# Kernel optimization log

Measured on AMD Instinct MI355X. Metric: run time of the kernel, lower is better.

The kernel has to match this reference:

```python
import jax, jax.numpy as jnp
import numpy as np

B, T, D, H, DK = 4, 1024, 512, 8, 64
L = 2 * T - 1  # relative position length
EPS = 1e-3     # keras LayerNormalization default epsilon


def rel_shift(x, klen):
    # x: [B, H, T, L] with L = 2T-1 -> [B, H, T, klen] (Transformer-XL shift)
    b, h, t, l = x.shape
    x = x.reshape(b, h, l, t)[:, :, 1:, :]
    x = x.reshape(b, h, t, l - 1)
    return x[:, :, :, :klen]


def setup_inputs() -> dict:
    key = jax.random.key(0)
    ks = jax.random.split(key, 16)
    s = 0.02
    return {
        "x": jax.random.normal(ks[0], (B, T, D), jnp.float32),
        "pos": jax.random.normal(ks[1], (B, L, D), jnp.float32),
        "content_bias": jax.random.normal(ks[2], (H, DK), jnp.float32) * s,
        "pos_bias": jax.random.normal(ks[3], (H, DK), jnp.float32) * s,
        "gamma": jnp.ones((D,), jnp.float32),
        "beta": jnp.zeros((D,), jnp.float32),
        "Wq": jax.random.normal(ks[4], (D, H, DK), jnp.float32) * s,
        "bq": jnp.zeros((H, DK), jnp.float32),
        "Wk": jax.random.normal(ks[5], (D, H, DK), jnp.float32) * s,
        "bk": jnp.zeros((H, DK), jnp.float32),
        "Wv": jax.random.normal(ks[6], (D, H, DK), jnp.float32) * s,
        "bv": jnp.zeros((H, DK), jnp.float32),
        "Wp": jax.random.normal(ks[7], (D, H, DK), jnp.float32) * s,
        "Wo": jax.random.normal(ks[8], (H, DK, D), jnp.float32) * s,
        "bo": jnp.zeros((D,), jnp.float32),
    }


def reference(x, pos, content_bias, pos_bias, gamma, beta,
              Wq, bq, Wk, bk, Wv, bv, Wp, Wo, bo):
    # pre-norm LayerNorm
    mean = jnp.mean(x, axis=-1, keepdims=True)
    var = jnp.var(x, axis=-1, keepdims=True)
    y = (x - mean) * jax.lax.rsqrt(var + EPS) * gamma + beta

    # per-head projections
    q = jnp.einsum("bid,dhk->bihk", y, Wq) + bq      # [B,T,H,DK]
    k = jnp.einsum("bjd,dhk->bjhk", y, Wk) + bk
    v = jnp.einsum("bjd,dhk->bjhk", y, Wv) + bv
    p = jnp.einsum("bld,dhk->blhk", pos, Wp)          # [B,L,H,DK], no bias

    # Transformer-XL content + positional scores
    content = jnp.einsum("bihk,bjhk->bhij", q + content_bias, k)   # [B,H,T,T]
    positional = jnp.einsum("bihk,blhk->bhil", q + pos_bias, p)    # [B,H,T,L]
    positional = rel_shift(positional, content.shape[-1])          # [B,H,T,T]

    scores = (content + positional) / np.sqrt(DK).astype(np.float32)
    attn = jax.nn.softmax(scores, axis=-1)

    o = jnp.einsum("bhij,bjhk->bihk", attn, v)       # [B,T,H,DK]
    out = jnp.einsum("bihk,hkd->bid", o, Wo) + bo    # [B,T,D]

    # dropout is identity at inference; residual with factor=1.0
    return x + out
```

## Files before the change

### kernel.cpp

```cpp
#include <hip/hip_runtime.h>
#include <hip/hip_bf16.h>

typedef __hip_bfloat16 bf16;
typedef __attribute__((ext_vector_type(8))) short short8;
typedef __attribute__((ext_vector_type(4))) float f32x4;

#define B_  4
#define T_  1024
#define D_  512
#define H_  8
#define DK_ 64
#define L_  2047

__device__ __forceinline__ float b2f(bf16 v) { return __bfloat162float(v); }
__device__ __forceinline__ bf16  f2b(float v) { return __float2bfloat16(v); }
__device__ __forceinline__ float bits2f(unsigned short u) {
    return __uint_as_float(((unsigned int)u) << 16);
}
__device__ __forceinline__ unsigned short fbits(float v) {
    bf16 h = f2b(v); return *(unsigned short*)&h;
}

#define MFMA16(a, b, c) __builtin_amdgcn_mfma_f32_16x16x32_bf16(a, b, c, 0, 0, 0)
#define GLD_LDS16(g, l) __builtin_amdgcn_global_load_lds( \
    (const __attribute__((address_space(1))) unsigned int*)(g), \
    (__attribute__((address_space(3))) unsigned int*)(l), 16, 0, 0)

__global__ __launch_bounds__(256) void prep_all(
        const float* __restrict__ Wq, const float* __restrict__ Wk,
        const float* __restrict__ Wv, const float* __restrict__ Wp,
        const float* __restrict__ Wo,
        const float* __restrict__ bq, const float* __restrict__ bk,
        const float* __restrict__ bv,
        const float* __restrict__ pos, const float* __restrict__ x,
        const float* __restrict__ gamma, const float* __restrict__ beta,
        bf16* __restrict__ Wqkv_t, bf16* __restrict__ Wp_t, bf16* __restrict__ Wo_t,
        float* __restrict__ biasq, bf16* __restrict__ pos_bf, bf16* __restrict__ y) {
    __shared__ float tl[32][33];
    __shared__ float ws1[4], ws2[4];
    const int blk = blockIdx.x;
    const int t = threadIdx.x;

    if (blk < 1280) {
        const int z = blk >> 8, rem = blk & 255;
        const float* W; bf16* Wt; int roff;
        switch (z) {
            case 0: W = Wq; Wt = Wqkv_t; roff = 0;    break;
            case 1: W = Wk; Wt = Wqkv_t; roff = 512;  break;
            case 2: W = Wv; Wt = Wqkv_t; roff = 1024; break;
            case 3: W = Wp; Wt = Wp_t;   roff = 0;    break;
            default: W = Wo; Wt = Wo_t;  roff = 0;    break;
        }
        const int n0 = (rem & 15) * 32, k0 = (rem >> 4) * 32;
        const int tx = t & 31, ty = t >> 5;
#pragma unroll
        for (int r = 0; r < 4; ++r)
            tl[ty + r * 8][tx] = W[(size_t)(k0 + ty + r * 8) * 512 + n0 + tx];
        __syncthreads();
#pragma unroll
        for (int r = 0; r < 4; ++r)
            Wt[(size_t)(roff + n0 + ty + r * 8) * 512 + k0 + tx] = f2b(tl[tx][ty + r * 8]);
    } else if (blk < 1286) {
        int i = (blk - 1280) * 256 + t;
        biasq[i] = (i < 512) ? bq[i] : (i < 1024) ? bk[i - 512] : bv[i - 1024];
    } else if (blk < 3333) {
        size_t i = ((size_t)(blk - 1286) * 256 + t) * 8;
        float4 a = *(const float4*)(pos + i);
        float4 c = *(const float4*)(pos + i + 4);
        uint4 wv;
        wv.x = ((unsigned)fbits(a.y) << 16) | fbits(a.x);
        wv.y = ((unsigned)fbits(a.w) << 16) | fbits(a.z);
        wv.z = ((unsigned)fbits(c.y) << 16) | fbits(c.x);
        wv.w = ((unsigned)fbits(c.w) << 16) | fbits(c.z);
        *(uint4*)((unsigned short*)pos_bf + i) = wv;
    } else {
        const int row = blk - 3333;
        const float* xr = x + (size_t)row * D_;
        float v0 = xr[t];
        float v1 = xr[t + 256];
        float s  = v0 + v1;
        float s2 = v0 * v0 + v1 * v1;
#pragma unroll
        for (int off = 32; off > 0; off >>= 1) {
            s  += __shfl_down(s,  off, 64);
            s2 += __shfl_down(s2, off, 64);
        }
        const int wid = t >> 6, lane = t & 63;
        if (!lane) { ws1[wid] = s; ws2[wid] = s2; }
        __syncthreads();
        float S  = ws1[0] + ws1[1] + ws1[2] + ws1[3];
        float S2 = ws2[0] + ws2[1] + ws2[2] + ws2[3];
        float mean = S * (1.f / D_);
        float var  = S2 * (1.f / D_) - mean * mean;
        float r = rsqrtf(var + 1e-3f);
        bf16* yr = y + (size_t)row * D_;
        yr[t]       = f2b((v0 - mean) * r * gamma[t]       + beta[t]);
        yr[t + 256] = f2b((v1 - mean) * r * gamma[t + 256] + beta[t + 256]);
    }
}

template <bool C_F32>
__device__ __forceinline__ void gemm_body(
        const bf16* __restrict__ A, const bf16* __restrict__ Wt,
        const float* __restrict__ bias, const float* __restrict__ resid,
        void* __restrict__ Cv, int M, size_t seg_elems, int m0, int n0,
        unsigned short (*A_s)[32], unsigned short (*B_s)[32]) {
    const int t = threadIdx.x;
    const int w = t >> 6, lane = t & 63;
    const int quad = lane >> 4, n16 = lane & 15;
    const int wm = (w >> 1) * 64, wn = (w & 1) * 64;

    f32x4 acc[4][4];
#pragma unroll
    for (int a = 0; a < 4; ++a)
#pragma unroll
        for (int b = 0; b < 4; ++b) acc[a][b] = (f32x4){0.f, 0.f, 0.f, 0.f};

    const int ar = lane >> 2, ac8 = (lane & 3) * 8;
    auto stage = [&](int k0, int buf) {
        const int bo = buf << 7;
#pragma unroll
        for (int ps = 0; ps < 2; ++ps) {
            int br = (ps * 4 + w) * 16;
            GLD_LDS16(A  + (size_t)(m0 + br + ar) * 512 + k0 + ac8, &A_s[bo + br][0]);
            GLD_LDS16(Wt + (size_t)(n0 + br + ar) * 512 + k0 + ac8, &B_s[bo + br][0]);
        }
    };
    stage(0, 0);
    int cur = 0;
    for (int k0 = 0; k0 < 512; k0 += 32) {
        __syncthreads();
        if (k0 + 32 < 512) stage(k0 + 32, cur ^ 1);
        const int bo = cur << 7;
        short8 af[4], bfr[4];
#pragma unroll
        for (int i = 0; i < 4; ++i) {
            af[i]  = *(const short8*)&A_s[bo + wm + i * 16 + n16][quad * 8];
            bfr[i] = *(const short8*)&B_s[bo + wn + i * 16 + n16][quad * 8];
        }
#pragma unroll
        for (int mi = 0; mi < 4; ++mi)
#pragma unroll
            for (int ni = 0; ni < 4; ++ni)
                acc[mi][ni] = MFMA16(af[mi], bfr[ni], acc[mi][ni]);
        cur ^= 1;
    }

    const int seg = n0 >> 9;
#pragma unroll
    for (int mi = 0; mi < 4; ++mi) {
#pragma unroll
        for (int r = 0; r < 4; ++r) {
            int row = m0 + wm + mi * 16 + quad * 4 + r;
            if (row >= M) continue;
#pragma unroll
            for (int ni = 0; ni < 4; ++ni) {
                int col  = n0 + wn + ni * 16 + n16;
                int coll = col & 511;
                float vv = acc[mi][ni][r];
                if (bias) vv += bias[col];
                if constexpr (C_F32) {
                    float* C = (float*)Cv + seg * seg_elems;
                    if (resid) vv += resid[(size_t)row * 512 + coll];
                    C[(size_t)row * 512 + coll] = vv;
                } else {
                    bf16* C = (bf16*)Cv + seg * seg_elems;
                    C[(size_t)row * 512 + coll] = f2b(vv);
                }
            }
        }
    }
}

__global__ __launch_bounds__(256) void gemm_qkvp(
        const bf16* __restrict__ y, const bf16* __restrict__ pos_bf,
        const bf16* __restrict__ Wqkv_t, const bf16* __restrict__ Wp_t,
        const float* __restrict__ biasq,
        bf16* __restrict__ q, bf16* __restrict__ p, size_t seg_elems) {
    __shared__ __align__(16) unsigned short A_s[256][32];
    __shared__ __align__(16) unsigned short B_s[256][32];
    const int gid = blockIdx.x;
    if (gid < 384) {
        const int xcd = gid & 7, s = gid >> 3;
        const int n = s % 12;
        const int m = xcd * 4 + s / 12;
        gemm_body<false>(y, Wqkv_t, biasq, nullptr, q, 4096, seg_elems,
                         m * 128, n * 128, A_s, B_s);
    } else {
        const int g2 = gid - 384;
        const int xcd = g2 & 7, s = g2 >> 3;
        const int n = s & 3;
        const int m = xcd * 8 + (s >> 2);
        gemm_body<false>(pos_bf, Wp_t, nullptr, nullptr, p, 8188, 0,
                         m * 128, n * 128, A_s, B_s);
    }
}

__global__ __launch_bounds__(256) void gemm_out(
        const bf16* __restrict__ o, const bf16* __restrict__ Wo_t,
        const float* __restrict__ bo, const float* __restrict__ x,
        float* __restrict__ out) {
    __shared__ __align__(16) unsigned short A_s[256][32];
    __shared__ __align__(16) unsigned short B_s[256][32];
    const int xcd = blockIdx.x & 7, s = blockIdx.x >> 3;
    const int n = s & 3;
    const int m = xcd * 4 + (s >> 2);
    gemm_body<true>(o, Wo_t, bo, x, out, 4096, 0, m * 128, n * 128, A_s, B_s);
}

__global__ __launch_bounds__(256, 2) void attn_mfma_kernel(
        const bf16* __restrict__ q, const bf16* __restrict__ k,
        const bf16* __restrict__ v, const bf16* __restrict__ p,
        const float* __restrict__ cbias, const float* __restrict__ pbias,
        bf16* __restrict__ o) {
    __shared__ __align__(16) unsigned short k_s[2][4096];
    __shared__ __align__(16) unsigned short pw_s[2][8192];
    __shared__ __align__(16) unsigned short vt_s[2][64][72];
    __shared__ __align__(16) unsigned short gbuf[4][16][72];
    __shared__ float cb_s[64], pb_s[64];
    __shared__ float wrap_s;

    const int i0 = blockIdx.x * 64;
    const int h  = blockIdx.y;
    const int b  = blockIdx.z;
    const int t  = threadIdx.x;
    const int w    = t >> 6;
    const int lane = t & 63;
    const int quad = lane >> 4;
    const int n16  = lane & 15;
    const int h64  = h * 64;
    const float sc_scale = 0.125f * 1.4426950408889634f;

    if (t < 64)       cb_s[t]      = cbias[h64 + t];
    else if (t < 128) pb_s[t - 64] = pbias[h64 + t - 64];

    const int l8 = lane >> 3, l7 = lane & 7;
    const int clog8 = (l7 ^ l8) * 8;
    const unsigned short* ksrc[2];
    const unsigned short* psrc[4];
#pragma unroll
    for (int ps = 0; ps < 2; ++ps) {
        int row = (w * 2 + ps) * 8 + l8;
        ksrc[ps] = (const unsigned short*)k + ((size_t)(b * T_ + row) * 512 + h64 + clog8);
    }
    const int slb = T_ - i0 - 63;
#pragma unroll
    for (int ps = 0; ps < 4; ++ps) {
        int row = (w * 4 + ps) * 8 + l8;
        psrc[ps] = (const unsigned short*)p + ((size_t)(b * L_ + slb + row) * 512 + h64 + clog8);
    }
    auto stage = [&](int j0n, int nxt) {
        size_t joff = (size_t)j0n * 512;
#pragma unroll
        for (int ps = 0; ps < 2; ++ps)
            GLD_LDS16(ksrc[ps] + joff, &k_s[nxt][(w * 2 + ps) * 512]);
#pragma unroll
        for (int ps = 0; ps < 4; ++ps)
            GLD_LDS16(psrc[ps] + joff, &pw_s[nxt][(w * 4 + ps) * 512]);
    };

    const int vd2 = (t & 31) * 2, vjg = t >> 5;
    const unsigned short* vsrc = (const unsigned short*)v +
        ((size_t)(b * T_ + vjg * 8) * 512 + h64 + vd2);
    unsigned int vReg[8];
    auto vload = [&](int j0n) {
        const unsigned short* vg = vsrc + (size_t)j0n * 512;
#pragma unroll
        for (int e = 0; e < 8; ++e) vReg[e] = *(const unsigned int*)(vg + (size_t)e * 512);
    };
    auto vwrite = [&](int nxt) {
        uint4 wlo, whi;
        wlo.x = (vReg[0] & 0xffffu) | (vReg[1] << 16);
        wlo.y = (vReg[2] & 0xffffu) | (vReg[3] << 16);
        wlo.z = (vReg[4] & 0xffffu) | (vReg[5] << 16);
        wlo.w = (vReg[6] & 0xffffu) | (vReg[7] << 16);
        whi.x = (vReg[0] >> 16) | (vReg[1] & 0xffff0000u);
        whi.y = (vReg[2] >> 16) | (vReg[3] & 0xffff0000u);
        whi.z = (vReg[4] >> 16) | (vReg[5] & 0xffff0000u);
        whi.w = (vReg[6] >> 16) | (vReg[7] & 0xffff0000u);
        *(uint4*)&vt_s[nxt][vd2][vjg * 8]     = wlo;
        *(uint4*)&vt_s[nxt][vd2 + 1][vjg * 8] = whi;
    };

    stage(0, 0);
    vload(0);
    __syncthreads();

    short8 ac[2], ap[2];
    {
        const unsigned short* qrow = (const unsigned short*)q +
            ((size_t)(b * T_ + i0 + 16 * w + n16) * 512 + h64);
#pragma unroll
        for (int kc = 0; kc < 2; ++kc) {
            uint4 u = *(const uint4*)(qrow + kc * 32 + quad * 8);
            const unsigned short* uv = (const unsigned short*)&u;
            unsigned short* acp = (unsigned short*)&ac[kc];
            unsigned short* app = (unsigned short*)&ap[kc];
#pragma unroll
            for (int e = 0; e < 8; ++e) {
                int d = kc * 32 + quad * 8 + e;
                float qv = bits2f(uv[e]);
                acp[e] = fbits((qv + cb_s[d]) * sc_scale);
                app[e] = fbits((qv + pb_s[d]) * sc_scale);
            }
        }
    }
    if (i0 == 0 && t < 64) {
        float part = (b2f(q[(size_t)(b * T_ + 1) * 512 + h64 + t]) + pb_s[t]) *
                     b2f(p[(size_t)(b * L_) * 512 + h64 + t]);
#pragma unroll
        for (int m = 1; m < 64; m <<= 1) part += __shfl_xor(part, m, 64);
        if (t == 0) wrap_s = part * sc_scale;
    }

    int srcl[4]; bool hi_[4];
#pragma unroll
    for (int r = 0; r < 4; ++r) {
        int ii = quad * 4 + r;
        srcl[r] = (lane & 48) | ((n16 - ii - 1) & 15);
        hi_[r]  = n16 > ii;
    }
    short8 onesb;
    {
        const short ov = (n16 == 0) ? (short)0x3F80 : (short)0;
#pragma unroll
        for (int e = 0; e < 8; ++e) onesb[e] = ov;
    }

    const int pwoff = 48 - 16 * w;
    const int swzA  = (quad ^ (n16 & 7)) * 16;
    const int swzB  = swzA ^ 64;

    f32x4 O[4], O4;
#pragma unroll
    for (int nt = 0; nt < 4; ++nt) O[nt] = (f32x4){0.f, 0.f, 0.f, 0.f};
    O4 = (f32x4){0.f, 0.f, 0.f, 0.f};

    auto qk = [&](f32x4 (&Sc)[4], f32x4 (&G)[5], int buf) {
        const char* krA  = (const char*)&k_s[buf][0]  + n16 * 128 + swzA;
        const char* krB  = (const char*)&k_s[buf][0]  + n16 * 128 + swzB;
        const char* pwrA = (const char*)&pw_s[buf][0] + (pwoff + n16) * 128 + swzA;
        const char* pwrB = (const char*)&pw_s[buf][0] + (pwoff + n16) * 128 + swzB;
#pragma unroll
        for (int nt = 0; nt < 4; ++nt) Sc[nt] = (f32x4){0.f, 0.f, 0.f, 0.f};
#pragma unroll
        for (int ct = 0; ct < 5; ++ct) G[ct] = (f32x4){0.f, 0.f, 0.f, 0.f};
#pragma unroll
        for (int kc = 0; kc < 2; ++kc) {
#pragma unroll
            for (int nt = 0; nt < 4; ++nt) {
                short8 bk = *(const short8*)((kc ? krB : krA) + nt * 2048);
                Sc[nt] = MFMA16(ac[kc], bk, Sc[nt]);
            }
#pragma unroll
            for (int ct = 0; ct < 5; ++ct) {
                short8 bp = *(const short8*)((kc ? pwrB : pwrA) + ct * 2048);
                G[ct] = MFMA16(ap[kc], bp, G[ct]);
            }
        }
    };

    auto sm_pv = [&](const f32x4 (&Sc)[4], const f32x4 (&G)[5], int vb, bool dowrap) {
        float pe[4][4];
#pragma unroll
        for (int r = 0; r < 4; ++r) {
            float s0 = __shfl(G[0][r], srcl[r], 64);
            float s1 = __shfl(G[1][r], srcl[r], 64);
            float s2 = __shfl(G[2][r], srcl[r], 64);
            float s3 = __shfl(G[3][r], srcl[r], 64);
            float s4 = __shfl(G[4][r], srcl[r], 64);
            pe[0][r] = Sc[0][r] + (hi_[r] ? s1 : s0);
            pe[1][r] = Sc[1][r] + (hi_[r] ? s2 : s1);
            pe[2][r] = Sc[2][r] + (hi_[r] ? s3 : s2);
            pe[3][r] = Sc[3][r] + (hi_[r] ? s4 : s3);
        }
        if (dowrap && i0 == 0 && w == 0 && lane == 15)
            pe[3][0] = Sc[3][0] + wrap_s;
#pragma unroll
        for (int ct = 0; ct < 4; ++ct)
#pragma unroll
            for (int r = 0; r < 4; ++r)
                *(bf16*)&gbuf[w][quad * 4 + r][ct * 16 + n16] = f2b(exp2f(pe[ct][r]));
#pragma unroll
        for (int kc = 0; kc < 2; ++kc) {
            short8 pa = *(const short8*)&gbuf[w][n16][kc * 32 + quad * 8];
#pragma unroll
            for (int nt = 0; nt < 4; ++nt) {
                short8 vb8 = *(const short8*)&vt_s[vb][nt * 16 + n16][kc * 32 + quad * 8];
                O[nt] = MFMA16(pa, vb8, O[nt]);
            }
            O4 = MFMA16(pa, onesb, O4);
        }
    };

    f32x4 ScA[4], GA[5], ScB[4], GB[5];

    vwrite(0);
    stage(64, 1);
    vload(64);
    qk(ScA, GA, 0);

    auto body = [&](int tt, f32x4 (&ScC)[4], f32x4 (&GC)[5],
                    const f32x4 (&ScP)[4], const f32x4 (&GP)[5], bool more) {
        __syncthreads();
        vwrite(tt & 1);
        if (more) { stage((tt + 1) * 64, (tt + 1) & 1); vload((tt + 1) * 64); }
        qk(ScC, GC, tt & 1);
        sm_pv(ScP, GP, (tt - 1) & 1, false);
    };

#pragma unroll
    for (int tp = 0; tp < 7; ++tp) {
        body(2 * tp + 1, ScB, GB, ScA, GA, true);
        body(2 * tp + 2, ScA, GA, ScB, GB, true);
    }
    body(15, ScB, GB, ScA, GA, false);

    __syncthreads();
    sm_pv(ScB, GB, 1, true);

#pragma unroll
    for (int r = 0; r < 4; ++r) {
        float l = __shfl(O4[r], lane & 48, 64);
        float inv = 1.f / l;
        int row = i0 + 16 * w + quad * 4 + r;
#pragma unroll
        for (int nt = 0; nt < 4; ++nt)
            o[(size_t)(b * T_ + row) * 512 + h64 + nt * 16 + n16] = f2b(O[nt][r] * inv);
    }
}

extern "C" void kernel_launch(void* const* d_in, const int* in_sizes, int n_in,
                              void* d_out, int out_size, void* d_ws, size_t ws_size,
                              hipStream_t stream) {
    (void)in_sizes; (void)n_in; (void)out_size;
    const float* x     = (const float*)d_in[0];
    const float* pos   = (const float*)d_in[1];
    const float* cb    = (const float*)d_in[2];
    const float* pb    = (const float*)d_in[3];
    const float* gamma = (const float*)d_in[4];
    const float* beta  = (const float*)d_in[5];
    const float* Wq    = (const float*)d_in[6];
    const float* bq    = (const float*)d_in[7];
    const float* Wk    = (const float*)d_in[8];
    const float* bk    = (const float*)d_in[9];
    const float* Wv    = (const float*)d_in[10];
    const float* bv    = (const float*)d_in[11];
    const float* Wp    = (const float*)d_in[12];
    const float* Wo    = (const float*)d_in[13];
    const float* bo    = (const float*)d_in[14];
    float* out = (float*)d_out;

    const int BT = B_ * T_;

    const size_t sz_bt = (size_t)BT * D_;
    const size_t sz_bl = (size_t)(B_ * L_) * D_;
    const size_t sz_w  = 512 * 512;
    const size_t need  = (5 * sz_bt + sz_bl + 5 * sz_w) * sizeof(bf16) + 1536 * sizeof(float);
    if (ws_size < need) return;

    bf16* y       = (bf16*)d_ws;
    bf16* o       = y + sz_bt;
    bf16* q       = y + 2 * sz_bt;
    bf16* k       = y + 3 * sz_bt;
    bf16* v       = y + 4 * sz_bt;
    bf16* p       = y + 5 * sz_bt;
    bf16* Wqkv_t  = p + sz_bl;
    bf16* Wp_t    = Wqkv_t + 3 * sz_w;
    bf16* Wo_t    = Wp_t + sz_w;
    float* biasq  = (float*)(Wo_t + sz_w);
    bf16* pos_bf  = (bf16*)d_out;

    prep_all<<<7429, 256, 0, stream>>>(Wq, Wk, Wv, Wp, Wo, bq, bk, bv, pos, x,
                                       gamma, beta, Wqkv_t, Wp_t, Wo_t, biasq, pos_bf, y);

    gemm_qkvp<<<640, 256, 0, stream>>>(y, pos_bf, Wqkv_t, Wp_t, biasq, q, p, sz_bt);

    attn_mfma_kernel<<<dim3(T_ / 64, H_, B_), 256, 0, stream>>>(q, k, v, p, cb, pb, o);

    gemm_out<<<128, 256, 0, stream>>>(o, Wo_t, bo, x, out);
}
```

Measured before the change: 208.4 us.

## Reuse overlapping positional tiles via ring buffer, retile output GEMM, add MFMA priority

Result: faster. 185.7 us (-10.9%).

```diff
diff --git a/kernel.cpp b/kernel.cpp
--- a/kernel.cpp
+++ b/kernel.cpp
@@ -99,11 +99,10 @@
     }
 }
 
-template <bool C_F32>
 __device__ __forceinline__ void gemm_body(
         const bf16* __restrict__ A, const bf16* __restrict__ Wt,
-        const float* __restrict__ bias, const float* __restrict__ resid,
-        void* __restrict__ Cv, int M, size_t seg_elems, int m0, int n0,
+        const float* __restrict__ bias,
+        bf16* __restrict__ C, int M, size_t seg_elems, int m0, int n0,
         unsigned short (*A_s)[32], unsigned short (*B_s)[32]) {
     const int t = threadIdx.x;
     const int w = t >> 6, lane = t & 63;
@@ -159,14 +158,8 @@
                 int coll = col & 511;
                 float vv = acc[mi][ni][r];
                 if (bias) vv += bias[col];
-                if constexpr (C_F32) {
-                    float* C = (float*)Cv + seg * seg_elems;
-                    if (resid) vv += resid[(size_t)row * 512 + coll];
-                    C[(size_t)row * 512 + coll] = vv;
-                } else {
-                    bf16* C = (bf16*)Cv + seg * seg_elems;
-                    C[(size_t)row * 512 + coll] = f2b(vv);
-                }
+                bf16* Cp = C + seg * seg_elems;
+                Cp[(size_t)row * 512 + coll] = f2b(vv);
             }
         }
     }
@@ -184,15 +177,13 @@
         const int xcd = gid & 7, s = gid >> 3;
         const int n = s % 12;
         const int m = xcd * 4 + s / 12;
-        gemm_body<false>(y, Wqkv_t, biasq, nullptr, q, 4096, seg_elems,
-                         m * 128, n * 128, A_s, B_s);
+        gemm_body(y, Wqkv_t, biasq, q, 4096, seg_elems, m * 128, n * 128, A_s, B_s);
     } else {
         const int g2 = gid - 384;
         const int xcd = g2 & 7, s = g2 >> 3;
         const int n = s & 3;
         const int m = xcd * 8 + (s >> 2);
-        gemm_body<false>(pos_bf, Wp_t, nullptr, nullptr, p, 8188, 0,
-                         m * 128, n * 128, A_s, B_s);
+        gemm_body(pos_bf, Wp_t, nullptr, p, 8188, 0, m * 128, n * 128, A_s, B_s);
     }
 }
 
@@ -200,12 +191,64 @@
         const bf16* __restrict__ o, const bf16* __restrict__ Wo_t,
         const float* __restrict__ bo, const float* __restrict__ x,
         float* __restrict__ out) {
-    __shared__ __align__(16) unsigned short A_s[256][32];
+    __shared__ __align__(16) unsigned short A_s[128][32];
     __shared__ __align__(16) unsigned short B_s[256][32];
-    const int xcd = blockIdx.x & 7, s = blockIdx.x >> 3;
-    const int n = s & 3;
-    const int m = xcd * 4 + (s >> 2);
-    gemm_body<true>(o, Wo_t, bo, x, out, 4096, 0, m * 128, n * 128, A_s, B_s);
+    const int gid = blockIdx.x;
+    const int xcd = gid & 7, s = gid >> 3;
+    const int n0 = (s & 3) * 128;
+    const int m0 = (xcd * 8 + (s >> 2)) * 64;
+    const int t = threadIdx.x;
+    const int w = t >> 6, lane = t & 63;
+    const int quad = lane >> 4, n16 = lane & 15;
+    const int wm = (w >> 1) * 32, wn = (w & 1) * 64;
+
+    f32x4 acc[2][4];
+#pragma unroll
+    for (int a = 0; a < 2; ++a)
+#pragma unroll
+        for (int b = 0; b < 4; ++b) acc[a][b] = (f32x4){0.f, 0.f, 0.f, 0.f};
+
+    const int ar = lane >> 2, ac8 = (lane & 3) * 8;
+    auto stage = [&](int k0, int buf) {
+        GLD_LDS16(o + (size_t)(m0 + w * 16 + ar) * 512 + k0 + ac8,
+                  &A_s[buf * 64 + w * 16][0]);
+#pragma unroll
+        for (int ps = 0; ps < 2; ++ps)
+            GLD_LDS16(Wo_t + (size_t)(n0 + (ps * 4 + w) * 16 + ar) * 512 + k0 + ac8,
+                      &B_s[buf * 128 + (ps * 4 + w) * 16][0]);
+    };
+    stage(0, 0);
+    int cur = 0;
+    for (int k0 = 0; k0 < 512; k0 += 32) {
+        __syncthreads();
+        if (k0 + 32 < 512) stage(k0 + 32, cur ^ 1);
+        short8 af[2], bfr[4];
+#pragma unroll
+        for (int i = 0; i < 2; ++i)
+            af[i] = *(const short8*)&A_s[cur * 64 + wm + i * 16 + n16][quad * 8];
+#pragma unroll
+        for (int i = 0; i < 4; ++i)
+            bfr[i] = *(const short8*)&B_s[cur * 128 + wn + i * 16 + n16][quad * 8];
+#pragma unroll
+        for (int mi = 0; mi < 2; ++mi)
+#pragma unroll
+            for (int ni = 0; ni < 4; ++ni)
+                acc[mi][ni] = MFMA16(af[mi], bfr[ni], acc[mi][ni]);
+        cur ^= 1;
+    }
+#pragma unroll
+    for (int mi = 0; mi < 2; ++mi) {
+#pragma unroll
+        for (int r = 0; r < 4; ++r) {
+            int row = m0 + wm + mi * 16 + quad * 4 + r;
+#pragma unroll
+            for (int ni = 0; ni < 4; ++ni) {
+                int col = n0 + wn + ni * 16 + n16;
+                out[(size_t)row * 512 + col] =
+                    acc[mi][ni][r] + bo[col] + x[(size_t)row * 512 + col];
+            }
+        }
+    }
 }
 
 __global__ __launch_bounds__(256, 2) void attn_mfma_kernel(
@@ -214,7 +257,7 @@
         const float* __restrict__ cbias, const float* __restrict__ pbias,
         bf16* __restrict__ o) {
     __shared__ __align__(16) unsigned short k_s[2][4096];
-    __shared__ __align__(16) unsigned short pw_s[2][8192];
+    __shared__ __align__(16) unsigned short pw_s[3][4096];
     __shared__ __align__(16) unsigned short vt_s[2][64][72];
     __shared__ __align__(16) unsigned short gbuf[4][16][72];
     __shared__ float cb_s[64], pb_s[64];
@@ -237,7 +280,7 @@
     const int l8 = lane >> 3, l7 = lane & 7;
     const int clog8 = (l7 ^ l8) * 8;
     const unsigned short* ksrc[2];
-    const unsigned short* psrc[4];
+    const unsigned short* psrc[2];
 #pragma unroll
     for (int ps = 0; ps < 2; ++ps) {
         int row = (w * 2 + ps) * 8 + l8;
@@ -245,18 +288,22 @@
     }
     const int slb = T_ - i0 - 63;
 #pragma unroll
-    for (int ps = 0; ps < 4; ++ps) {
-        int row = (w * 4 + ps) * 8 + l8;
+    for (int ps = 0; ps < 2; ++ps) {
+        int row = (w * 2 + ps) * 8 + l8;
         psrc[ps] = (const unsigned short*)p + ((size_t)(b * L_ + slb + row) * 512 + h64 + clog8);
     }
-    auto stage = [&](int j0n, int nxt) {
-        size_t joff = (size_t)j0n * 512;
+    auto stageP = [&](int c) {
+        size_t joff = (size_t)c * 64 * 512;
 #pragma unroll
         for (int ps = 0; ps < 2; ++ps)
-            GLD_LDS16(ksrc[ps] + joff, &k_s[nxt][(w * 2 + ps) * 512]);
-#pragma unroll
-        for (int ps = 0; ps < 4; ++ps)
-            GLD_LDS16(psrc[ps] + joff, &pw_s[nxt][(w * 4 + ps) * 512]);
+            GLD_LDS16(psrc[ps] + joff, &pw_s[c % 3][(w * 2 + ps) * 512]);
+    };
+    auto stage = [&](int n) {
+        size_t joff = (size_t)n * 64 * 512;
+#pragma unroll
+        for (int ps = 0; ps < 2; ++ps)
+            GLD_LDS16(ksrc[ps] + joff, &k_s[n & 1][(w * 2 + ps) * 512]);
+        stageP(n + 1);
     };
 
     const int vd2 = (t & 31) * 2, vjg = t >> 5;
@@ -282,7 +329,8 @@
         *(uint4*)&vt_s[nxt][vd2 + 1][vjg * 8] = whi;
     };
 
-    stage(0, 0);
+    stageP(0);
+    stage(0);
     vload(0);
     __syncthreads();
 
@@ -327,24 +375,25 @@
         for (int e = 0; e < 8; ++e) onesb[e] = ov;
     }
 
-    const int pwoff = 48 - 16 * w;
-    const int swzA  = (quad ^ (n16 & 7)) * 16;
-    const int swzB  = swzA ^ 64;
+    const int swzA = (quad ^ (n16 & 7)) * 16;
+    const int swzB = swzA ^ 64;
 
     f32x4 O[4], O4;
 #pragma unroll
     for (int nt = 0; nt < 4; ++nt) O[nt] = (f32x4){0.f, 0.f, 0.f, 0.f};
     O4 = (f32x4){0.f, 0.f, 0.f, 0.f};
 
-    auto qk = [&](f32x4 (&Sc)[4], f32x4 (&G)[5], int buf) {
-        const char* krA  = (const char*)&k_s[buf][0]  + n16 * 128 + swzA;
-        const char* krB  = (const char*)&k_s[buf][0]  + n16 * 128 + swzB;
-        const char* pwrA = (const char*)&pw_s[buf][0] + (pwoff + n16) * 128 + swzA;
-        const char* pwrB = (const char*)&pw_s[buf][0] + (pwoff + n16) * 128 + swzB;
+    auto qk = [&](f32x4 (&Sc)[4], f32x4 (&G)[5], int tn) {
+        const int buf = tn & 1;
+        const char* krA = (const char*)&k_s[buf][0] + n16 * 128 + swzA;
+        const char* krB = (const char*)&k_s[buf][0] + n16 * 128 + swzB;
+        const char* pbank[2] = { (const char*)&pw_s[tn % 3][0],
+                                 (const char*)&pw_s[(tn + 1) % 3][0] };
 #pragma unroll
         for (int nt = 0; nt < 4; ++nt) Sc[nt] = (f32x4){0.f, 0.f, 0.f, 0.f};
 #pragma unroll
         for (int ct = 0; ct < 5; ++ct) G[ct] = (f32x4){0.f, 0.f, 0.f, 0.f};
+        __builtin_amdgcn_s_setprio(1);
 #pragma unroll
         for (int kc = 0; kc < 2; ++kc) {
 #pragma unroll
@@ -354,10 +403,14 @@
             }
 #pragma unroll
             for (int ct = 0; ct < 5; ++ct) {
-                short8 bp = *(const short8*)((kc ? pwrB : pwrA) + ct * 2048);
+                const int gi = 3 - w + ct;
+                const char* pr = pbank[gi >> 2] +
+                    ((gi & 3) * 16 + n16) * 128 + (kc ? swzB : swzA);
+                short8 bp = *(const short8*)pr;
                 G[ct] = MFMA16(ap[kc], bp, G[ct]);
             }
         }
+        __builtin_amdgcn_s_setprio(0);
     };
 
     auto sm_pv = [&](const f32x4 (&Sc)[4], const f32x4 (&G)[5], int vb, bool dowrap) {
@@ -381,6 +434,7 @@
 #pragma unroll
             for (int r = 0; r < 4; ++r)
                 *(bf16*)&gbuf[w][quad * 4 + r][ct * 16 + n16] = f2b(exp2f(pe[ct][r]));
+        __builtin_amdgcn_s_setprio(1);
 #pragma unroll
         for (int kc = 0; kc < 2; ++kc) {
             short8 pa = *(const short8*)&gbuf[w][n16][kc * 32 + quad * 8];
@@ -391,12 +445,13 @@
             }
             O4 = MFMA16(pa, onesb, O4);
         }
+        __builtin_amdgcn_s_setprio(0);
     };
 
     f32x4 ScA[4], GA[5], ScB[4], GB[5];
 
     vwrite(0);
-    stage(64, 1);
+    stage(1);
     vload(64);
     qk(ScA, GA, 0);
 
@@ -404,8 +459,8 @@
                     const f32x4 (&ScP)[4], const f32x4 (&GP)[5], bool more) {
         __syncthreads();
         vwrite(tt & 1);
-        if (more) { stage((tt + 1) * 64, (tt + 1) & 1); vload((tt + 1) * 64); }
-        qk(ScC, GC, tt & 1);
+        if (more) { stage(tt + 1); vload((tt + 1) * 64); }
+        qk(ScC, GC, tt);
         sm_pv(ScP, GP, (tt - 1) & 1, false);
     };
 
@@ -478,5 +533,5 @@
 
     attn_mfma_kernel<<<dim3(T_ / 64, H_, B_), 256, 0, stream>>>(q, k, v, p, cb, pb, o);
 
-    gemm_out<<<128, 256, 0, stream>>>(o, Wo_t, bo, x, out);
-}
+    gemm_out<<<256, 256, 0, stream>>>(o, Wo_t, bo, x, out);
+}
```
